# Performance work log

Hardware: AMD Instinct MI355X
Metric: run time of the kernel (lower is better)

Reference implementation:

```python
import jax, jax.numpy as jnp
import numpy as np

N, T, D, H = 128, 128, 1024, 1024


def setup_inputs() -> dict:
    key = jax.random.key(0)
    ks = jax.random.split(key, 5)
    x = jax.random.normal(ks[0], (N, T, D), dtype=jnp.float32)
    A = jax.random.normal(ks[1], (N, H, 4, 4), dtype=jnp.float32)
    Wx = jax.random.normal(ks[2], (D, 4 * H), dtype=jnp.float32) / np.sqrt(D)
    Wh = jax.random.normal(ks[3], (H, 4 * H), dtype=jnp.float32) / np.sqrt(H)
    Wattn = jax.random.normal(ks[4], (H, 4 * H), dtype=jnp.float32) / np.sqrt(H)
    b = jnp.zeros((4 * H,), dtype=jnp.float32)
    return {"x": x, "A": A, "Wx": Wx, "Wh": Wh, "Wattn": Wattn, "b": b}


def reference(x, A, Wx, Wh, Wattn, b):
    n, t, d = x.shape
    h_dim = A.shape[1]
    scale = 1.0 / (h_dim ** 0.5)
    A_flat = A.reshape(n, h_dim, 16)            # (N, H, 16) flattened 4x4 grid
    h0 = A_flat.mean(axis=2)                    # mean-pooled feature init
    c0 = h0

    def step(carry, xt):
        h, c = carry
        # scaled dot-product attention over the 16 spatial positions
        scores = jnp.einsum('nh,nhp->np', h, A_flat) * scale   # (N, 16)
        w = jax.nn.softmax(scores, axis=-1)
        attn = jnp.einsum('nhp,np->nh', A_flat, w)             # (N, H)
        # fused gate pre-activations
        a = h @ Wh + xt @ Wx + attn @ Wattn + b                # (N, 4H)
        ai, af, ao, ag = jnp.split(a, 4, axis=1)
        i = jax.nn.sigmoid(ai)
        f = jax.nn.sigmoid(af)
        o = jax.nn.sigmoid(ao)
        g = jnp.tanh(ag)
        nc = f * c + i * g
        nh = o * jnp.tanh(nc)
        return (nh, nc), nh

    _, hs = jax.lax.scan(step, (h0, c0), jnp.transpose(x, (1, 0, 2)))
    return jnp.transpose(hs, (1, 0, 2))         # (N, T, H)
```

## Files before the change

### kernel.cpp

```cpp
#include <hip/hip_runtime.h>
#include <hip/hip_bf16.h>


typedef __bf16 bf16x8 __attribute__((ext_vector_type(8)));
typedef float f32x4 __attribute__((ext_vector_type(4)));

__device__ __forceinline__ unsigned short f2bf(float f) {
    unsigned int u = __float_as_uint(f);
    u += 0x7FFFu + ((u >> 16) & 1u);
    return (unsigned short)(u >> 16);
}
__device__ __forceinline__ float bf2f(unsigned short u) {
    return __uint_as_float(((unsigned int)u) << 16);
}
__device__ __forceinline__ float sigf(float x) { return 1.0f / (1.0f + __expf(-x)); }
__device__ __forceinline__ float tanhf_fast(float x) {
    const float t = __expf(-2.0f * fabsf(x));
    const float r = (1.0f - t) / (1.0f + t);
    return copysignf(r, x);
}

__global__ __launch_bounds__(256) void k_build_wtf2(
    const float* __restrict__ Wh, const float* __restrict__ Wx,
    unsigned short* __restrict__ WTf) {
    __shared__ float tile[64][65];
    const int cs2 = blockIdx.x;
    const int kq  = blockIdx.y;
    const int tid = threadIdx.x;
#pragma unroll
    for (int it = 0; it < 16; ++it) {
        int idx = it * 256 + tid;
        int kl = idx >> 6, cl = idx & 63;
        int col = cs2 * 64 + cl;
        int j = (col & 3) * 1024 + (col >> 2);
        int k = kq * 64 + kl;
        tile[kl][cl] = (k < 1024) ? Wh[(size_t)k * 4096 + j]
                                  : Wx[(size_t)(k - 1024) * 4096 + j];
    }
    __syncthreads();
#pragma unroll
    for (int it = 0; it < 2; ++it) {
        int slotid = it * 256 + tid;
        int l   = slotid & 63;
        int cf  = (slotid >> 6) & 1;
        int ksl = (slotid >> 7) & 1;
        int sl  = slotid >> 8;
        int s = cs2 * 2 + sl, ks = kq * 2 + ksl;
        int clocal = sl * 32 + cf * 16 + (l & 15);
        int klocal = ksl * 32 + ((l >> 4) << 3);
        unsigned short v[8];
#pragma unroll
        for (int i = 0; i < 8; ++i) v[i] = f2bf(tile[klocal + i][clocal]);
        *(int4*)&WTf[(size_t)(((s * 64 + ks) * 2 + cf) * 64 + l) * 8] = *(const int4*)v;
    }
}

__global__ __launch_bounds__(256) void k_build_waf(
    const float* __restrict__ Wattn, unsigned short* __restrict__ WAf) {
    __shared__ float tile[64][65];
    const int cs2 = blockIdx.x;
    const int kq  = blockIdx.y;
    const int tid = threadIdx.x;
#pragma unroll
    for (int it = 0; it < 16; ++it) {
        int idx = it * 256 + tid;
        int kl = idx >> 6, cl = idx & 63;
        int col = cs2 * 64 + cl;
        int j = (col & 3) * 1024 + (col >> 2);
        int k = kq * 64 + kl;
        tile[kl][cl] = Wattn[(size_t)k * 4096 + j];
    }
    __syncthreads();
#pragma unroll
    for (int it = 0; it < 2; ++it) {
        int slotid = it * 256 + tid;
        int l   = slotid & 63;
        int cf  = (slotid >> 6) & 1;
        int ksl = (slotid >> 7) & 1;
        int sl  = slotid >> 8;
        int s = cs2 * 2 + sl, ks = kq * 2 + ksl;
        int clocal = sl * 32 + cf * 16 + (l & 15);
        int klocal = ksl * 32 + ((l >> 4) << 3);
        unsigned short v[8];
#pragma unroll
        for (int i = 0; i < 8; ++i) v[i] = f2bf(tile[klocal + i][clocal]);
        *(int4*)&WAf[(size_t)(((s * 32 + ks) * 2 + cf) * 64 + l) * 8] = *(const int4*)v;
    }
}

__global__ __launch_bounds__(256) void k_pack_at(
    const float* __restrict__ Ag, unsigned short* __restrict__ ATf) {
    __shared__ unsigned short lds[1024][17];
    const int n = blockIdx.x;
    const int tid = threadIdx.x;
#pragma unroll
    for (int it = 0; it < 16; ++it) {
        int idx = it * 256 + tid;
        const float4 v = ((const float4*)(Ag + (size_t)n * 16384))[idx];
        int flat = idx * 4;
        int u = flat >> 4, p = flat & 15;
        lds[u][p + 0] = f2bf(v.x); lds[u][p + 1] = f2bf(v.y);
        lds[u][p + 2] = f2bf(v.z); lds[u][p + 3] = f2bf(v.w);
    }
    __syncthreads();
#pragma unroll
    for (int it = 0; it < 8; ++it) {
        int slot = it * 256 + tid;
        int kc = slot >> 6, l = slot & 63;
        int ubase = kc * 32 + ((l >> 4) << 3);
        int p = l & 15;
        unsigned short v[8];
#pragma unroll
        for (int i = 0; i < 8; ++i) v[i] = lds[ubase + i][p];
        *(int4*)&ATf[((size_t)n * 2048 + slot) * 8] = *(const int4*)v;
    }
}

__global__ __launch_bounds__(512) void k_aw_gemm(
    const unsigned short* __restrict__ ATf, const unsigned short* __restrict__ WAf,
    unsigned short* __restrict__ AW) {
    const int ng = blockIdx.x;
    const int ct = blockIdx.y;
    const int tid = threadIdx.x;
    const int lane = tid & 63, wave = tid >> 6;
    const int s = ct * 4 + (wave >> 1), cf = wave & 1;
    const int n0 = ng * 8;
    f32x4 acc[8] = {};
    const unsigned short* bp = WAf + ((size_t)((s * 32) * 2 + cf) * 64 + lane) * 8;
    const unsigned short* ap = ATf + ((size_t)n0 * 2048 + lane) * 8;
#pragma unroll 4
    for (int kc = 0; kc < 32; ++kc) {
        bf16x8 bf = *(const bf16x8*)(bp + (size_t)kc * 1024);
#pragma unroll
        for (int nn = 0; nn < 8; ++nn) {
            bf16x8 af = *(const bf16x8*)(ap + (size_t)nn * 16384 + (size_t)kc * 512);
            acc[nn] = __builtin_amdgcn_mfma_f32_16x16x32_bf16(af, bf, acc[nn], 0, 0, 0);
        }
    }
    const int col = ct * 128 + wave * 16 + (lane & 15);
    const int prow = (lane >> 4) << 2;
#pragma unroll
    for (int nn = 0; nn < 8; ++nn) {
        ushort4 st = make_ushort4(f2bf(acc[nn][0]), f2bf(acc[nn][1]),
                                  f2bf(acc[nn][2]), f2bf(acc[nn][3]));
        *(ushort4*)&AW[((size_t)(n0 + nn) * 4096 + col) * 16 + prow] = st;
    }
}

__global__ __launch_bounds__(512) void k_build_aw(
    const float* __restrict__ Wattn, const float* __restrict__ Ag,
    unsigned short* __restrict__ AW) {
    extern __shared__ float Alds[];
    const int jt = blockIdx.x;
    const int ng = blockIdx.y;
    const int tid = threadIdx.x;
    const int jl = tid & 127, pg = tid >> 7;
    const int jj = jt * 128 + jl;
    for (int nn = 0; nn < 16; ++nn) {
        const int n = ng * 16 + nn;
        __syncthreads();
#pragma unroll
        for (int q = 0; q < 8; ++q) {
            int idx = q * 512 + tid;
            ((float4*)Alds)[idx] = ((const float4*)(Ag + (size_t)n * 16384))[idx];
        }
        __syncthreads();
        f32x4 acc = {0.f, 0.f, 0.f, 0.f};
#pragma unroll 8
        for (int u = 0; u < 1024; ++u) {
            float wv = Wattn[(size_t)u * 4096 + jj];
            const float4 av = *(const float4*)&Alds[u * 16 + pg * 4];
            acc[0] += wv * av.x; acc[1] += wv * av.y;
            acc[2] += wv * av.z; acc[3] += wv * av.w;
        }
        const int g = jj >> 10, unit = jj & 1023;
        const int cre = unit * 4 + g;
        ushort4 st = make_ushort4(f2bf(acc[0]), f2bf(acc[1]), f2bf(acc[2]), f2bf(acc[3]));
        *(ushort4*)&AW[((size_t)n * 4096 + cre) * 16 + pg * 4] = st;
    }
}

__global__ __launch_bounds__(512) void k_init(
    const float* __restrict__ Ag, float* __restrict__ cst,
    unsigned short* __restrict__ hF0, float* __restrict__ sp) {
    const int n = blockIdx.x;
    const int t = threadIdx.x;
    float contrib[16];
#pragma unroll
    for (int p = 0; p < 16; ++p) contrib[p] = 0.f;
#pragma unroll
    for (int e = 0; e < 2; ++e) {
        const int u = t * 2 + e;
        const float4* ap = (const float4*)&Ag[((size_t)n * 1024 + u) * 16];
        float4 a0 = ap[0], a1 = ap[1], a2 = ap[2], a3 = ap[3];
        float s = a0.x + a0.y + a0.z + a0.w + a1.x + a1.y + a1.z + a1.w +
                  a2.x + a2.y + a2.z + a2.w + a3.x + a3.y + a3.z + a3.w;
        float h0 = s * (1.0f / 16.0f);
        cst[n * 1024 + u] = h0;
        const int rfg = n >> 4, kc = u >> 5, l = (n & 15) | (((u >> 3) & 3) << 4);
        hF0[(size_t)((rfg * 32 + kc) * 64 + l) * 8 + (u & 7)] = f2bf(h0);
        contrib[0]  += h0 * a0.x;  contrib[1]  += h0 * a0.y;
        contrib[2]  += h0 * a0.z;  contrib[3]  += h0 * a0.w;
        contrib[4]  += h0 * a1.x;  contrib[5]  += h0 * a1.y;
        contrib[6]  += h0 * a1.z;  contrib[7]  += h0 * a1.w;
        contrib[8]  += h0 * a2.x;  contrib[9]  += h0 * a2.y;
        contrib[10] += h0 * a2.z;  contrib[11] += h0 * a2.w;
        contrib[12] += h0 * a3.x;  contrib[13] += h0 * a3.y;
        contrib[14] += h0 * a3.z;  contrib[15] += h0 * a3.w;
    }
#pragma unroll
    for (int p = 0; p < 16; ++p) {
        contrib[p] += __shfl_xor(contrib[p], 1);
        contrib[p] += __shfl_xor(contrib[p], 2);
    }
    if ((t & 3) == 0) {
        const int slice = t >> 2;
        float4* dst = (float4*)&sp[(size_t)n * 4096 + slice * 16];
        dst[0] = make_float4(contrib[0], contrib[1], contrib[2], contrib[3]);
        dst[1] = make_float4(contrib[4], contrib[5], contrib[6], contrib[7]);
        dst[2] = make_float4(contrib[8], contrib[9], contrib[10], contrib[11]);
        dst[3] = make_float4(contrib[12], contrib[13], contrib[14], contrib[15]);
    }
    *(float4*)&sp[(size_t)n * 4096 + 2048 + t * 4] = make_float4(0.f, 0.f, 0.f, 0.f);
}

__global__ __launch_bounds__(64) void k_soft(
    const float* __restrict__ spin, float* __restrict__ w_ws,
    const float* __restrict__ x, unsigned short* __restrict__ xf, int ts) {
    __shared__ float sq[16];
    const int n = blockIdx.x;
    const int lane = threadIdx.x;
    f32x4 acc = {0.f, 0.f, 0.f, 0.f};
    const float4* base = (const float4*)(spin + (size_t)n * 4096);
#pragma unroll
    for (int it = 0; it < 16; ++it) {
        const float4 v = base[it * 64 + lane];
        acc[0] += v.x; acc[1] += v.y; acc[2] += v.z; acc[3] += v.w;
    }
#pragma unroll
    for (int m = 4; m <= 32; m <<= 1) {
        acc[0] += __shfl_xor(acc[0], m);
        acc[1] += __shfl_xor(acc[1], m);
        acc[2] += __shfl_xor(acc[2], m);
        acc[3] += __shfl_xor(acc[3], m);
    }
    if (lane < 4) *(float4*)&sq[lane * 4] = make_float4(acc[0], acc[1], acc[2], acc[3]);
    __syncthreads();
    if (lane < 16) {
        const float s = sq[lane] * 0.03125f;
        float mx = s;
#pragma unroll
        for (int m = 1; m < 16; m <<= 1) mx = fmaxf(mx, __shfl_xor(mx, m));
        const float e = __expf(s - mx);
        float se = e;
#pragma unroll
        for (int m = 1; m < 16; m <<= 1) se += __shfl_xor(se, m);
        w_ws[n * 16 + lane] = e / se;
    }
    const float4* xp = (const float4*)&x[((size_t)n * 128 + ts) * 1024];
#pragma unroll
    for (int i = 0; i < 2; ++i) {
        const int js = lane * 2 + i;
        const float4 x0 = xp[js * 2], x1 = xp[js * 2 + 1];
        unsigned short v[8] = {f2bf(x0.x), f2bf(x0.y), f2bf(x0.z), f2bf(x0.w),
                               f2bf(x1.x), f2bf(x1.y), f2bf(x1.z), f2bf(x1.w)};
        const int j0 = js * 8;
        const int l = (n & 15) | (((j0 >> 3) & 3) << 4);
        *(int4*)&xf[(size_t)(((n >> 4) * 32 + (j0 >> 5)) * 64 + l) * 8] = *(const int4*)v;
    }
}

__global__ __launch_bounds__(512, 4) void k_step(
    const unsigned short* __restrict__ WTf, const unsigned short* __restrict__ AW,
    const unsigned short* __restrict__ hFin, unsigned short* __restrict__ hFout,
    const unsigned short* __restrict__ xf,
    const float* __restrict__ w_ws, float* __restrict__ spout,
    float* __restrict__ cst, const float* __restrict__ Ag,
    const float* __restrict__ bias4, float* __restrict__ out, int ts) {
    __shared__ float wlds[64][17];
    __shared__ float accred[2048];
    const int bid0 = blockIdx.x;
    const int lid = (bid0 & 7) * 64 + (bid0 >> 3);
    const int cs16 = lid >> 1, rh = lid & 1;
    const int tid = threadIdx.x;
    const int lane = tid & 63, wave = tid >> 6;
    const int rf = wave >> 1, kh = wave & 1;

    f32x4 acc = {0.f, 0.f, 0.f, 0.f};
    {
        const unsigned short* ap = (kh == 0 ? hFin : xf)
            + ((size_t)((rh * 4 + rf) * 32) * 64 + lane) * 8;
        const unsigned short* bp = WTf
            + ((size_t)((((cs16 >> 1) * 64 + kh * 32) * 2) + (cs16 & 1)) * 64 + lane) * 8;
        bf16x8 ar[8], br[8];
#pragma unroll
        for (int i = 0; i < 8; ++i) {
            ar[i] = *(const bf16x8*)(ap + (size_t)i * 512);
            br[i] = *(const bf16x8*)(bp + (size_t)i * 1024);
        }
#pragma unroll
        for (int kb = 0; kb < 32; ++kb) {
            bf16x8 a = ar[kb & 7], b = br[kb & 7];
            if (kb < 24) {
                ar[kb & 7] = *(const bf16x8*)(ap + (size_t)(kb + 8) * 512);
                br[kb & 7] = *(const bf16x8*)(bp + (size_t)(kb + 8) * 1024);
            }
            acc = __builtin_amdgcn_mfma_f32_16x16x32_bf16(a, b, acc, 0, 0, 0);
        }
    }

    const int lq = lane & 15;
    const int hi = lane >> 4;
    const int mycol = cs16 * 16 + lq;
    const int u = mycol >> 2, g = mycol & 3;
    int4 aw0[2], aw1[2];
    float cold[2];
#pragma unroll
    for (int e = 0; e < 2; ++e) {
        const int reg = kh * 2 + e;
        const int r = rh * 64 + rf * 16 + hi * 4 + reg;
        const int4* awv = (const int4*)&AW[((size_t)r * 4096 + mycol) * 16];
        aw0[e] = awv[0];
        aw1[e] = awv[1];
        cold[e] = cst[r * 1024 + u];
    }
#pragma unroll
    for (int it = 0; it < 2; ++it) {
        const int idx = it * 512 + tid;
        wlds[idx >> 4][idx & 15] = w_ws[(rh * 64 + (idx >> 4)) * 16 + (idx & 15)];
    }
    *(f32x4*)&accred[(wave * 64 + lane) * 4] = acc;
    __syncthreads();
    acc += *(const f32x4*)&accred[(((rf << 1) | (kh ^ 1)) * 64 + lane) * 4];

    const float bias = bias4[g * 1024 + u];
    float nhv[2];
#pragma unroll
    for (int e = 0; e < 2; ++e) {
        const int reg = kh * 2 + e;
        const int r = rh * 64 + rf * 16 + hi * 4 + reg;
        const int rl = rf * 16 + hi * 4 + reg;
        union { int4 v; unsigned short us[8]; } a0u, a1u;
        a0u.v = aw0[e]; a1u.v = aw1[e];
        float aextra = 0.f;
#pragma unroll
        for (int p = 0; p < 8; ++p) aextra += wlds[rl][p] * bf2f(a0u.us[p]);
#pragma unroll
        for (int p = 0; p < 8; ++p) aextra += wlds[rl][8 + p] * bf2f(a1u.us[p]);
        float a = acc[reg] + bias + aextra;
        float v1 = __shfl_xor(a, 1);
        float v2 = __shfl_xor(a, 2);
        float v3 = __shfl_xor(a, 3);
        auto pick = [&](int m) { return m == 0 ? a : m == 1 ? v1 : m == 2 ? v2 : v3; };
        float ii = sigf(pick(g));
        float ff = sigf(pick(g ^ 1));
        float oo = sigf(pick(g ^ 2));
        float gg = tanhf_fast(pick(g ^ 3));
        const float nc = ff * cold[e] + ii * gg;
        const float nh = oo * tanhf_fast(nc);
        nhv[e] = nh;
        if (g == 0) {
            cst[r * 1024 + u] = nc;
        } else if (g == 1) {
            hFout[(size_t)(((r >> 4) * 32 + (u >> 5)) * 64 +
                           ((r & 15) | (((u >> 3) & 3) << 4))) * 8 + (u & 7)] = f2bf(nh);
        } else if (g == 3) {
            out[((size_t)r * 128 + ts) * 1024 + u] = nh;
        }
    }
    if ((lq & 3) == 2) {
#pragma unroll
        for (int e = 0; e < 2; ++e) {
            const int reg = kh * 2 + e;
            const int r = rh * 64 + rf * 16 + hi * 4 + reg;
            const float nh = nhv[e];
            const float4* Ap = (const float4*)&Ag[((size_t)r * 1024 + u) * 16];
            float contrib[16];
#pragma unroll
            for (int q = 0; q < 4; ++q) {
                const float4 cv = Ap[q];
                contrib[q * 4 + 0] = nh * cv.x;
                contrib[q * 4 + 1] = nh * cv.y;
                contrib[q * 4 + 2] = nh * cv.z;
                contrib[q * 4 + 3] = nh * cv.w;
            }
#pragma unroll
            for (int p = 0; p < 16; ++p) {
                contrib[p] += __shfl_xor(contrib[p], 4);
                contrib[p] += __shfl_xor(contrib[p], 8);
            }
            if (lq == 2) {
                float4* dst = (float4*)&spout[((size_t)r * 256 + cs16) * 16];
                dst[0] = make_float4(contrib[0], contrib[1], contrib[2], contrib[3]);
                dst[1] = make_float4(contrib[4], contrib[5], contrib[6], contrib[7]);
                dst[2] = make_float4(contrib[8], contrib[9], contrib[10], contrib[11]);
                dst[3] = make_float4(contrib[12], contrib[13], contrib[14], contrib[15]);
            }
        }
    }
}

extern "C" void kernel_launch(void* const* d_in, const int* in_sizes, int n_in,
                              void* d_out, int out_size, void* d_ws, size_t ws_size,
                              hipStream_t stream) {
    const float* x     = (const float*)d_in[0];
    const float* A     = (const float*)d_in[1];
    const float* Wx    = (const float*)d_in[2];
    const float* Wh    = (const float*)d_in[3];
    const float* Wattn = (const float*)d_in[4];
    const float* b     = (const float*)d_in[5];
    float* out = (float*)d_out;

    char* ws = (char*)d_ws;
    unsigned short* WTf = (unsigned short*)(ws);
    unsigned short* AW  = (unsigned short*)(ws + 16777216);
    unsigned short* hF0 = (unsigned short*)(ws + 33554432);
    unsigned short* hF1 = (unsigned short*)(ws + 33816576);
    unsigned short* xf  = (unsigned short*)(ws + 34078720);
    float* cst  = (float*)(ws + 34340864);
    float* w_ws = (float*)(ws + 34865152);
    float* sp0  = (float*)(ws + 34873344);
    float* sp1  = (float*)(ws + 36970496);
    unsigned short* ATf = (unsigned short*)(ws + 33554432);
    unsigned short* WAf = (unsigned short*)(ws + 37748736);

    k_build_wtf2<<<dim3(64, 32), 256, 0, stream>>>(Wh, Wx, WTf);
    if (ws_size >= 46137344u) {
        k_build_waf<<<dim3(64, 16), 256, 0, stream>>>(Wattn, WAf);
        k_pack_at<<<128, 256, 0, stream>>>(A, ATf);
        k_aw_gemm<<<dim3(16, 32), 512, 0, stream>>>(ATf, WAf, AW);
    } else {
        k_build_aw<<<dim3(32, 8), 512, 65536, stream>>>(Wattn, A, AW);
    }
    k_init<<<128, 512, 0, stream>>>(A, cst, hF0, sp0);

    for (int ts = 0; ts < 128; ++ts) {
        unsigned short* hin  = (ts & 1) ? hF1 : hF0;
        unsigned short* hout = (ts & 1) ? hF0 : hF1;
        float* spin  = (ts & 1) ? sp1 : sp0;
        float* spout = (ts & 1) ? sp0 : sp1;
        k_soft<<<128, 64, 0, stream>>>(spin, w_ws, x, xf, ts);
        k_step<<<512, 512, 0, stream>>>(WTf, AW, hin, hout, xf,
                                        w_ws, spout, cst, A, b, out, ts);
    }
}
```

Baseline: 2.661 ms.

## Fuse softmax into step kernel with flag sync and prefetch next x

```diff
diff --git a/kernel.cpp b/kernel.cpp
--- a/kernel.cpp
+++ b/kernel.cpp
@@ -55,8 +55,8 @@
     }
 }
 
-__global__ __launch_bounds__(256) void k_build_waf(
-    const float* __restrict__ Wattn, unsigned short* __restrict__ WAf) {
+__global__ __launch_bounds__(256) void k_build_wf(
+    const float* __restrict__ W, unsigned short* __restrict__ WF) {
     __shared__ float tile[64][65];
     const int cs2 = blockIdx.x;
     const int kq  = blockIdx.y;
@@ -68,7 +68,7 @@
         int col = cs2 * 64 + cl;
         int j = (col & 3) * 1024 + (col >> 2);
         int k = kq * 64 + kl;
-        tile[kl][cl] = Wattn[(size_t)k * 4096 + j];
+        tile[kl][cl] = W[(size_t)k * 4096 + j];
     }
     __syncthreads();
 #pragma unroll
@@ -84,7 +84,7 @@
         unsigned short v[8];
 #pragma unroll
         for (int i = 0; i < 8; ++i) v[i] = f2bf(tile[klocal + i][clocal]);
-        *(int4*)&WAf[(size_t)(((s * 32 + ks) * 2 + cf) * 64 + l) * 8] = *(const int4*)v;
+        *(int4*)&WF[(size_t)(((s * 32 + ks) * 2 + cf) * 64 + l) * 8] = *(const int4*)v;
     }
 }
 
@@ -181,10 +181,22 @@
 }
 
 __global__ __launch_bounds__(512) void k_init(
-    const float* __restrict__ Ag, float* __restrict__ cst,
-    unsigned short* __restrict__ hF0, float* __restrict__ sp) {
+    const float* __restrict__ Ag, const float* __restrict__ x,
+    float* __restrict__ cst, unsigned short* __restrict__ hF0,
+    unsigned short* __restrict__ xf0, float* __restrict__ sp,
+    int* __restrict__ flags) {
     const int n = blockIdx.x;
     const int t = threadIdx.x;
+    if (n == 0 && t < 128) flags[t] = 0;
+    if (t < 128) {
+        const int j0 = t * 8;
+        const float4* xp = (const float4*)&x[((size_t)n * 128 + 0) * 1024 + j0];
+        float4 x0 = xp[0], x1 = xp[1];
+        unsigned short v[8] = {f2bf(x0.x), f2bf(x0.y), f2bf(x0.z), f2bf(x0.w),
+                               f2bf(x1.x), f2bf(x1.y), f2bf(x1.z), f2bf(x1.w)};
+        const int rfg = n >> 4, kc = j0 >> 5, l = (n & 15) | (((j0 >> 3) & 3) << 4);
+        *(int4*)&xf0[(size_t)((rfg * 32 + kc) * 64 + l) * 8] = *(const int4*)v;
+    }
     float contrib[16];
 #pragma unroll
     for (int p = 0; p < 16; ++p) contrib[p] = 0.f;
@@ -224,130 +236,152 @@
     *(float4*)&sp[(size_t)n * 4096 + 2048 + t * 4] = make_float4(0.f, 0.f, 0.f, 0.f);
 }
 
-__global__ __launch_bounds__(64) void k_soft(
-    const float* __restrict__ spin, float* __restrict__ w_ws,
-    const float* __restrict__ x, unsigned short* __restrict__ xf, int ts) {
-    __shared__ float sq[16];
-    const int n = blockIdx.x;
-    const int lane = threadIdx.x;
-    f32x4 acc = {0.f, 0.f, 0.f, 0.f};
-    const float4* base = (const float4*)(spin + (size_t)n * 4096);
-#pragma unroll
-    for (int it = 0; it < 16; ++it) {
-        const float4 v = base[it * 64 + lane];
-        acc[0] += v.x; acc[1] += v.y; acc[2] += v.z; acc[3] += v.w;
-    }
-#pragma unroll
-    for (int m = 4; m <= 32; m <<= 1) {
-        acc[0] += __shfl_xor(acc[0], m);
-        acc[1] += __shfl_xor(acc[1], m);
-        acc[2] += __shfl_xor(acc[2], m);
-        acc[3] += __shfl_xor(acc[3], m);
-    }
-    if (lane < 4) *(float4*)&sq[lane * 4] = make_float4(acc[0], acc[1], acc[2], acc[3]);
-    __syncthreads();
-    if (lane < 16) {
-        const float s = sq[lane] * 0.03125f;
-        float mx = s;
-#pragma unroll
-        for (int m = 1; m < 16; m <<= 1) mx = fmaxf(mx, __shfl_xor(mx, m));
-        const float e = __expf(s - mx);
-        float se = e;
-#pragma unroll
-        for (int m = 1; m < 16; m <<= 1) se += __shfl_xor(se, m);
-        w_ws[n * 16 + lane] = e / se;
-    }
-    const float4* xp = (const float4*)&x[((size_t)n * 128 + ts) * 1024];
-#pragma unroll
-    for (int i = 0; i < 2; ++i) {
-        const int js = lane * 2 + i;
-        const float4 x0 = xp[js * 2], x1 = xp[js * 2 + 1];
-        unsigned short v[8] = {f2bf(x0.x), f2bf(x0.y), f2bf(x0.z), f2bf(x0.w),
-                               f2bf(x1.x), f2bf(x1.y), f2bf(x1.z), f2bf(x1.w)};
-        const int j0 = js * 8;
-        const int l = (n & 15) | (((j0 >> 3) & 3) << 4);
-        *(int4*)&xf[(size_t)(((n >> 4) * 32 + (j0 >> 5)) * 64 + l) * 8] = *(const int4*)v;
-    }
-}
-
 __global__ __launch_bounds__(512, 4) void k_step(
     const unsigned short* __restrict__ WTf, const unsigned short* __restrict__ AW,
     const unsigned short* __restrict__ hFin, unsigned short* __restrict__ hFout,
-    const unsigned short* __restrict__ xf,
-    const float* __restrict__ w_ws, float* __restrict__ spout,
-    float* __restrict__ cst, const float* __restrict__ Ag,
+    const unsigned short* __restrict__ xfin, unsigned short* __restrict__ xfout,
+    float* __restrict__ w_ws, int* __restrict__ sflag,
+    float* __restrict__ sp, float* __restrict__ cst,
+    const float* __restrict__ Ag, const float* __restrict__ x,
     const float* __restrict__ bias4, float* __restrict__ out, int ts) {
-    __shared__ float wlds[64][17];
-    __shared__ float accred[2048];
+    __shared__ float wlds[128][17];
     const int bid0 = blockIdx.x;
-    const int lid = (bid0 & 7) * 64 + (bid0 >> 3);
-    const int cs16 = lid >> 1, rh = lid & 1;
     const int tid = threadIdx.x;
     const int lane = tid & 63, wave = tid >> 6;
-    const int rf = wave >> 1, kh = wave & 1;
-
-    f32x4 acc = {0.f, 0.f, 0.f, 0.f};
+
+    if (bid0 >= 256) {
+        const int n = (bid0 - 256) * 8 + wave;
+        f32x4 acc = {0.f, 0.f, 0.f, 0.f};
+        const float4* base = (const float4*)(sp + (size_t)n * 4096);
+#pragma unroll
+        for (int it = 0; it < 16; ++it) {
+            const float4 v = base[it * 64 + lane];
+            acc[0] += v.x; acc[1] += v.y; acc[2] += v.z; acc[3] += v.w;
+        }
+#pragma unroll
+        for (int m = 4; m <= 32; m <<= 1) {
+            acc[0] += __shfl_xor(acc[0], m);
+            acc[1] += __shfl_xor(acc[1], m);
+            acc[2] += __shfl_xor(acc[2], m);
+            acc[3] += __shfl_xor(acc[3], m);
+        }
+        if (lane < 4) *(f32x4*)&wlds[wave][lane * 4] = acc;
+        __syncthreads();
+        if (lane < 16) {
+            const float s = wlds[wave][lane] * 0.03125f;
+            float mx = s;
+#pragma unroll
+            for (int m = 1; m < 16; m <<= 1) mx = fmaxf(mx, __shfl_xor(mx, m));
+            const float e = __expf(s - mx);
+            float se = e;
+#pragma unroll
+            for (int m = 1; m < 16; m <<= 1) se += __shfl_xor(se, m);
+            __hip_atomic_store(&w_ws[n * 16 + lane], e / se,
+                               __ATOMIC_RELAXED, __HIP_MEMORY_SCOPE_AGENT);
+        }
+        __syncthreads();
+        if (tid == 0) {
+            __threadfence();
+            atomicAdd(sflag, 1);
+        }
+        if (ts + 1 < 128) {
+#pragma unroll
+            for (int it = 0; it < 2; ++it) {
+                const int slot = it * 8192 + (bid0 - 256) * 512 + tid;
+                const int nn = slot >> 7, js = slot & 127, j0 = js * 8;
+                const float4* xp =
+                    (const float4*)&x[((size_t)nn * 128 + (ts + 1)) * 1024 + j0];
+                float4 x0 = xp[0], x1 = xp[1];
+                unsigned short v[8] = {f2bf(x0.x), f2bf(x0.y), f2bf(x0.z), f2bf(x0.w),
+                                       f2bf(x1.x), f2bf(x1.y), f2bf(x1.z), f2bf(x1.w)};
+                const int rfg = nn >> 4, kc = j0 >> 5,
+                          l = (nn & 15) | (((j0 >> 3) & 3) << 4);
+                *(int4*)&xfout[(size_t)((rfg * 32 + kc) * 64 + l) * 8] = *(const int4*)v;
+            }
+        }
+        return;
+    }
+
+    const int cs16 = (bid0 & 7) * 32 + (bid0 >> 3);
+
+    f32x4 acc2[2] = {};
     {
-        const unsigned short* ap = (kh == 0 ? hFin : xf)
-            + ((size_t)((rh * 4 + rf) * 32) * 64 + lane) * 8;
+        const unsigned short* aph = hFin + ((size_t)(wave * 32) * 64 + lane) * 8;
+        const unsigned short* apx = xfin + ((size_t)(wave * 32) * 64 + lane) * 8;
         const unsigned short* bp = WTf
-            + ((size_t)((((cs16 >> 1) * 64 + kh * 32) * 2) + (cs16 & 1)) * 64 + lane) * 8;
+            + ((size_t)(((cs16 >> 1) * 64) * 2 + (cs16 & 1)) * 64 + lane) * 8;
         bf16x8 ar[8], br[8];
 #pragma unroll
         for (int i = 0; i < 8; ++i) {
-            ar[i] = *(const bf16x8*)(ap + (size_t)i * 512);
+            ar[i] = *(const bf16x8*)(aph + (size_t)i * 512);
             br[i] = *(const bf16x8*)(bp + (size_t)i * 1024);
         }
 #pragma unroll
-        for (int kb = 0; kb < 32; ++kb) {
+        for (int kb = 0; kb < 64; ++kb) {
             bf16x8 a = ar[kb & 7], b = br[kb & 7];
-            if (kb < 24) {
-                ar[kb & 7] = *(const bf16x8*)(ap + (size_t)(kb + 8) * 512);
-                br[kb & 7] = *(const bf16x8*)(bp + (size_t)(kb + 8) * 1024);
+            if (kb < 56) {
+                const int ks = kb + 8;
+                ar[kb & 7] = (ks < 32)
+                    ? *(const bf16x8*)(aph + (size_t)ks * 512)
+                    : *(const bf16x8*)(apx + (size_t)(ks - 32) * 512);
+                br[kb & 7] = *(const bf16x8*)(bp + (size_t)ks * 1024);
             }
-            acc = __builtin_amdgcn_mfma_f32_16x16x32_bf16(a, b, acc, 0, 0, 0);
-        }
-    }
-
-    const int lq = lane & 15;
-    const int hi = lane >> 4;
+            acc2[kb >> 5] = __builtin_amdgcn_mfma_f32_16x16x32_bf16(a, b, acc2[kb >> 5], 0, 0, 0);
+        }
+    }
+    const f32x4 acc = acc2[0] + acc2[1];
+
+    const int lq = lane & 15, hi = lane >> 4;
     const int mycol = cs16 * 16 + lq;
     const int u = mycol >> 2, g = mycol & 3;
-    int4 aw0[2], aw1[2];
-    float cold[2];
-#pragma unroll
-    for (int e = 0; e < 2; ++e) {
-        const int reg = kh * 2 + e;
-        const int r = rh * 64 + rf * 16 + hi * 4 + reg;
+    const int r0 = wave * 16 + hi * 4;
+    int4 aw0[4], aw1[4];
+    float cold[4];
+#pragma unroll
+    for (int e = 0; e < 4; ++e) {
+        const int r = r0 + e;
         const int4* awv = (const int4*)&AW[((size_t)r * 4096 + mycol) * 16];
         aw0[e] = awv[0];
         aw1[e] = awv[1];
         cold[e] = cst[r * 1024 + u];
     }
-#pragma unroll
-    for (int it = 0; it < 2; ++it) {
-        const int idx = it * 512 + tid;
-        wlds[idx >> 4][idx & 15] = w_ws[(rh * 64 + (idx >> 4)) * 16 + (idx & 15)];
-    }
-    *(f32x4*)&accred[(wave * 64 + lane) * 4] = acc;
+    const float bias = bias4[g * 1024 + u];
+
+    if (tid == 0) {
+        while (__hip_atomic_load(sflag, __ATOMIC_ACQUIRE,
+                                 __HIP_MEMORY_SCOPE_AGENT) < 16) {
+            __builtin_amdgcn_s_sleep(2);
+        }
+    }
     __syncthreads();
-    acc += *(const f32x4*)&accred[(((rf << 1) | (kh ^ 1)) * 64 + lane) * 4];
-
-    const float bias = bias4[g * 1024 + u];
-    float nhv[2];
-#pragma unroll
-    for (int e = 0; e < 2; ++e) {
-        const int reg = kh * 2 + e;
-        const int r = rh * 64 + rf * 16 + hi * 4 + reg;
-        const int rl = rf * 16 + hi * 4 + reg;
+    {
+        const unsigned long long* wsrc = (const unsigned long long*)w_ws;
+#pragma unroll
+        for (int it = 0; it < 2; ++it) {
+            const int idx = it * 512 + tid;
+            const unsigned long long v = __hip_atomic_load(
+                &wsrc[idx], __ATOMIC_RELAXED, __HIP_MEMORY_SCOPE_AGENT);
+            union { unsigned long long q; float f[2]; } cv;
+            cv.q = v;
+            const int f0 = idx * 2;
+            wlds[f0 >> 4][f0 & 15] = cv.f[0];
+            wlds[f0 >> 4][(f0 & 15) + 1] = cv.f[1];
+        }
+    }
+    __syncthreads();
+
+    float nhv[4];
+#pragma unroll
+    for (int e = 0; e < 4; ++e) {
+        const int r = r0 + e;
         union { int4 v; unsigned short us[8]; } a0u, a1u;
         a0u.v = aw0[e]; a1u.v = aw1[e];
         float aextra = 0.f;
 #pragma unroll
-        for (int p = 0; p < 8; ++p) aextra += wlds[rl][p] * bf2f(a0u.us[p]);
-#pragma unroll
-        for (int p = 0; p < 8; ++p) aextra += wlds[rl][8 + p] * bf2f(a1u.us[p]);
-        float a = acc[reg] + bias + aextra;
+        for (int p = 0; p < 8; ++p) aextra += wlds[r][p] * bf2f(a0u.us[p]);
+#pragma unroll
+        for (int p = 0; p < 8; ++p) aextra += wlds[r][8 + p] * bf2f(a1u.us[p]);
+        float a = acc[e] + bias + aextra;
         float v1 = __shfl_xor(a, 1);
         float v2 = __shfl_xor(a, 2);
         float v3 = __shfl_xor(a, 3);
@@ -370,9 +404,8 @@
     }
     if ((lq & 3) == 2) {
 #pragma unroll
-        for (int e = 0; e < 2; ++e) {
-            const int reg = kh * 2 + e;
-            const int r = rh * 64 + rf * 16 + hi * 4 + reg;
+        for (int e = 0; e < 4; ++e) {
+            const int r = r0 + e;
             const float nh = nhv[e];
             const float4* Ap = (const float4*)&Ag[((size_t)r * 1024 + u) * 16];
             float contrib[16];
@@ -390,7 +423,7 @@
                 contrib[p] += __shfl_xor(contrib[p], 8);
             }
             if (lq == 2) {
-                float4* dst = (float4*)&spout[((size_t)r * 256 + cs16) * 16];
+                float4* dst = (float4*)&sp[((size_t)r * 256 + cs16) * 16];
                 dst[0] = make_float4(contrib[0], contrib[1], contrib[2], contrib[3]);
                 dst[1] = make_float4(contrib[4], contrib[5], contrib[6], contrib[7]);
                 dst[2] = make_float4(contrib[8], contrib[9], contrib[10], contrib[11]);
@@ -416,31 +449,32 @@
     unsigned short* AW  = (unsigned short*)(ws + 16777216);
     unsigned short* hF0 = (unsigned short*)(ws + 33554432);
     unsigned short* hF1 = (unsigned short*)(ws + 33816576);
-    unsigned short* xf  = (unsigned short*)(ws + 34078720);
-    float* cst  = (float*)(ws + 34340864);
-    float* w_ws = (float*)(ws + 34865152);
-    float* sp0  = (float*)(ws + 34873344);
-    float* sp1  = (float*)(ws + 36970496);
+    unsigned short* xfA = (unsigned short*)(ws + 34078720);
+    unsigned short* xfB = (unsigned short*)(ws + 34340864);
+    float* cst   = (float*)(ws + 34603008);
+    float* w_ws  = (float*)(ws + 35127296);
+    int*   flags = (int*)(ws + 35135488);
+    float* sp    = (float*)(ws + 35143680);
     unsigned short* ATf = (unsigned short*)(ws + 33554432);
     unsigned short* WAf = (unsigned short*)(ws + 37748736);
 
     k_build_wtf2<<<dim3(64, 32), 256, 0, stream>>>(Wh, Wx, WTf);
     if (ws_size >= 46137344u) {
-        k_build_waf<<<dim3(64, 16), 256, 0, stream>>>(Wattn, WAf);
+        k_build_wf<<<dim3(64, 16), 256, 0, stream>>>(Wattn, WAf);
         k_pack_at<<<128, 256, 0, stream>>>(A, ATf);
         k_aw_gemm<<<dim3(16, 32), 512, 0, stream>>>(ATf, WAf, AW);
     } else {
         k_build_aw<<<dim3(32, 8), 512, 65536, stream>>>(Wattn, A, AW);
     }
-    k_init<<<128, 512, 0, stream>>>(A, cst, hF0, sp0);
+    k_init<<<128, 512, 0, stream>>>(A, x, cst, hF0, xfA, sp, flags);
 
     for (int ts = 0; ts < 128; ++ts) {
         unsigned short* hin  = (ts & 1) ? hF1 : hF0;
         unsigned short* hout = (ts & 1) ? hF0 : hF1;
-        float* spin  = (ts & 1) ? sp1 : sp0;
-        float* spout = (ts & 1) ? sp0 : sp1;
-        k_soft<<<128, 64, 0, stream>>>(spin, w_ws, x, xf, ts);
-        k_step<<<512, 512, 0, stream>>>(WTf, AW, hin, hout, xf,
-                                        w_ws, spout, cst, A, b, out, ts);
-    }
-}
+        unsigned short* xin  = (ts & 1) ? xfB : xfA;
+        unsigned short* xout = (ts & 1) ? xfA : xfB;
+        k_step<<<272, 512, 0, stream>>>(WTf, AW, hin, hout, xin, xout,
+                                        w_ws, flags + ts, sp, cst,
+                                        A, x, b, out, ts);
+    }
+}
```

New measurement: 6.191 ms. 2.33x slower.
